# Optimization experiments

Hardware: AMD Instinct MI355X
Metric: run time of the kernel (lower is better)

The kernel has to match this reference:

```python
import jax, jax.numpy as jnp
import numpy as np

N = 100000      # nodes
E = 1600000     # edges
IN, H, OUT = 128, 128, 64
P_DROP = 0.5


def _glorot_linear(key, out_d, in_d):
    # PyG Linear default init (kaiming-uniform-ish); exact init is irrelevant for the baseline
    bound = 1.0 / np.sqrt(in_d)
    return jax.random.uniform(key, (out_d, in_d), jnp.float32, -bound, bound)


def setup_inputs() -> dict:
    key = jax.random.key(0)
    ks = jax.random.split(key, 8)
    x = jax.random.normal(ks[0], (N, IN), jnp.float32)
    edge_index = jax.random.randint(ks[1], (2, E), 0, N, dtype=jnp.int64)
    W1l = _glorot_linear(ks[2], H, IN)
    b1 = jnp.zeros((H,), jnp.float32)
    W1r = _glorot_linear(ks[3], H, IN)
    W2l = _glorot_linear(ks[4], OUT, H)
    b2 = jnp.zeros((OUT,), jnp.float32)
    W2r = _glorot_linear(ks[5], OUT, H)
    return dict(x=x, edge_index=edge_index, W1l=W1l, b1=b1, W1r=W1r,
                W2l=W2l, b2=b2, W2r=W2r)


def _sage_conv(x, src, dst, Wl, bl, Wr):
    # PyG SAGEConv (aggr='mean'): out = lin_l(mean_{j in N(i)} x_j) + lin_r(x_i)
    msg = x[src]                                             # [E, d] gather
    agg = jax.ops.segment_sum(msg, dst, num_segments=N)      # [N, d] scatter-add
    cnt = jax.ops.segment_sum(jnp.ones((src.shape[0], 1), x.dtype), dst,
                              num_segments=N)                # [N, 1] in-degree
    mean = agg / jnp.maximum(cnt, 1.0)                       # isolated nodes -> 0
    return mean @ Wl.T + bl + x @ Wr.T


def reference(x, edge_index, W1l, b1, W1r, W2l, b2, W2r):
    src, dst = edge_index[0], edge_index[1]
    h = _sage_conv(x, src, dst, W1l, b1, W1r)
    h = jax.nn.relu(h)
    # F.dropout(p=0.5) made deterministic with a fixed key
    keep = jax.random.bernoulli(jax.random.key(42), 1.0 - P_DROP, h.shape)
    h = jnp.where(keep, h / (1.0 - P_DROP), 0.0)
    return _sage_conv(h, src, dst, W2l, b2, W2r)
```

## Files before the change

kernel.cpp:

```cpp
#include <hip/hip_runtime.h>
#include <hip/hip_bf16.h>

#define N_NODES 100000
#define NE      1600000

#define BINSH 7
#define NBIN  782
#define BCAP  3072
#define SEPB  16384
#define SC_BLKS ((NE + SEPB - 1) / SEPB)
#define PRE_BLKS 512
#define NMASKW 200000

typedef __attribute__((ext_vector_type(8))) short bfrag;
typedef __attribute__((ext_vector_type(4))) float ffrag;

#define BFLO(u) __uint_as_float((u) << 16)
#define BFHI(u) __uint_as_float((u) & 0xffff0000u)

__device__ __forceinline__ unsigned tf_rotl(unsigned x, int d) {
    return (x << d) | (x >> (32 - d));
}

__device__ __forceinline__ unsigned tf_word(unsigned f) {
    const unsigned ks0 = 0u;
    const unsigned ks1 = 42u;
    const unsigned ks2 = 0x1BD11BDAu ^ 0u ^ 42u;
    unsigned x0 = 0u + ks0;
    unsigned x1 = f + ks1;
#define TF_RND(r) { x0 += x1; x1 = tf_rotl(x1, r); x1 ^= x0; }
    TF_RND(13) TF_RND(15) TF_RND(26) TF_RND(6)
    x0 += ks1; x1 += ks2 + 1u;
    TF_RND(17) TF_RND(29) TF_RND(16) TF_RND(24)
    x0 += ks2; x1 += ks0 + 2u;
    TF_RND(13) TF_RND(15) TF_RND(26) TF_RND(6)
    x0 += ks0; x1 += ks1 + 3u;
    TF_RND(17) TF_RND(29) TF_RND(16) TF_RND(24)
    x0 += ks1; x1 += ks2 + 4u;
    TF_RND(13) TF_RND(15) TF_RND(26) TF_RND(6)
    x0 += ks2; x1 += ks0 + 5u;
#undef TF_RND
    return x0 ^ x1;
}

__device__ __forceinline__ unsigned short bf_bits(float v) {
    __hip_bfloat16 b = __float2bfloat16(v);
    return *(unsigned short*)&b;
}

__global__ __launch_bounds__(1024) void k_prescatter(
    const int* __restrict__ ei, int* __restrict__ bincur, int* __restrict__ pairs,
    const float4* __restrict__ x4, ushort4* __restrict__ xb4,
    const float* __restrict__ W1l, const float* __restrict__ W1r,
    const float* __restrict__ W2l, const float* __restrict__ W2r,
    __hip_bfloat16* __restrict__ wb, unsigned long long* __restrict__ km) {
    const int t = threadIdx.x;

    if (blockIdx.x < SC_BLKS) {
        __shared__ int nz;
        __shared__ int h[NBIN];
        __shared__ int lbase[NBIN];
        if (t == 0) nz = 0;
        for (int i = t; i < NBIN; i += 1024) h[i] = 0;
        __syncthreads();
        if (t < 1024 && ei[2 * t + 1] != 0) atomicAdd(&nz, 1);
        __syncthreads();
        const int is64 = (nz == 0) ? 1 : 0;

        const int e0 = blockIdx.x * SEPB + t;
        int d[16], s[16];
#pragma unroll
        for (int k = 0; k < 16; ++k) {
            int e = e0 + k * 1024;
            if (e < NE) {
                d[k] = is64 ? ei[2 * (NE + e)] : ei[NE + e];
                s[k] = is64 ? ei[2 * e]        : ei[e];
                atomicAdd(&h[d[k] >> BINSH], 1);
            } else {
                d[k] = -1; s[k] = 0;
            }
        }
        __syncthreads();
        for (int i = t; i < NBIN; i += 1024) {
            int c = h[i];
            lbase[i] = c ? atomicAdd(&bincur[i], c) : 0;
            h[i] = 0;
        }
        __syncthreads();
#pragma unroll
        for (int k = 0; k < 16; ++k) {
            if (d[k] >= 0) {
                int b = d[k] >> BINSH;
                int r = atomicAdd(&h[b], 1);
                pairs[(size_t)b * BCAP + lbase[b] + r] =
                    ((d[k] & 127) << 17) | s[k];
            }
        }
    } else {
        const int tid0 = (blockIdx.x - SC_BLKS) * 1024 + t;
        const int stride = (PRE_BLKS - SC_BLKS) * 1024;
        for (int i = tid0; i < N_NODES * 128 / 4; i += stride) {
            float4 v = x4[i];
            ushort4 o;
            o.x = bf_bits(v.x); o.y = bf_bits(v.y);
            o.z = bf_bits(v.z); o.w = bf_bits(v.w);
            xb4[i] = o;
        }
        for (int i = tid0; i < 49152; i += stride) {
            float v;
            if (i < 16384)      v = W1l[i];
            else if (i < 32768) v = W1r[i - 16384];
            else if (i < 40960) v = W2l[i - 32768];
            else                v = W2r[i - 40960];
            wb[i] = __float2bfloat16(v);
        }
        const int lane = t & 63;
        const int gw = tid0 >> 6;
        const int nw = stride >> 6;
        for (int widx = gw; widx < NMASKW; widx += nw) {
            unsigned wv = tf_word((unsigned)widx * 64u + (unsigned)lane);
            unsigned long long keep = __ballot(!(wv & 0x80000000u));
            if (lane == 0) km[widx] = keep;
        }
    }
}

__global__ __launch_bounds__(1024) void k_aggcsr(
        const __hip_bfloat16* __restrict__ feat,
        const int* __restrict__ pairs, const int* __restrict__ bincnt,
        int* __restrict__ ptr, int* __restrict__ adj,
        __hip_bfloat16* __restrict__ mean) {
    __shared__ int ladj[BCAP];
    __shared__ int cnt[128];
    __shared__ int sc[128];
    __shared__ int woff[128];
    __shared__ int red[16];
    __shared__ int base_s;
    const int b = blockIdx.x >> 1;
    const int hb = blockIdx.x & 1;
    const int t = threadIdx.x;

    int s = 0;
    for (int i = t; i < b; i += 1024) s += bincnt[i];
#pragma unroll
    for (int off = 32; off > 0; off >>= 1) s += __shfl_down(s, off);
    if ((t & 63) == 0) red[t >> 6] = s;
    if (t < 128) cnt[t] = 0;
    __syncthreads();
    if (t == 0) {
        int tot = 0;
#pragma unroll
        for (int i = 0; i < 16; ++i) tot += red[i];
        base_s = tot;
    }
    __syncthreads();
    const int base = base_s;
    const int nb = bincnt[b];
    const int* pb = pairs + (size_t)b * BCAP;

    for (int i = t; i < nb; i += 1024)
        atomicAdd(&cnt[(pb[i] >> 17) & 127], 1);
    __syncthreads();
    if (t < 128) sc[t] = cnt[t];
    __syncthreads();
    for (int o = 1; o < 128; o <<= 1) {
        int u = 0;
        if (t < 128 && t >= o) u = sc[t - o];
        __syncthreads();
        if (t < 128) sc[t] += u;
        __syncthreads();
    }
    if (t < 128) {
        int ex = sc[t] - cnt[t];
        int node = b * 128 + t;
        if (hb == ((t >> 6) & 1) && node <= N_NODES) ptr[node] = base + ex;
        woff[t] = ex;
    }
    __syncthreads();
    for (int i = t; i < nb; i += 1024) {
        int pk = pb[i];
        int dl = (pk >> 17) & 127;
        if ((dl >> 6) == hb) {
            int r = atomicAdd(&woff[dl], 1);
            int src = pk & 0x1FFFF;
            ladj[r] = src;
            adj[base + r] = src;
        }
    }
    __syncthreads();

    const int w = t >> 6;
    const int l = t & 63;
    const int half = l >> 5;
    const size_t coff = (size_t)(l & 31) * 4;
    for (int i = 0; i < 4; ++i) {
        const int local = hb * 64 + w * 4 + i;
        const int node = b * 128 + local;
        if (node >= N_NODES) continue;
        const int p1 = sc[local];
        const int p0 = p1 - cnt[local];
        float c0 = 0.f, c1 = 0.f, c2 = 0.f, c3 = 0.f;
        float d0 = 0.f, d1 = 0.f, d2 = 0.f, d3 = 0.f;
        int p = p0;
        for (; p + 15 < p1; p += 16) {
            int sx[8];
#pragma unroll
            for (int k = 0; k < 8; ++k) sx[k] = ladj[p + 2 * k + half];
#pragma unroll
            for (int k = 0; k < 8; ++k) {
                uint2 u = *(const uint2*)(feat + (size_t)sx[k] * 128 + coff);
                if (k & 1) { d0 += BFLO(u.x); d1 += BFHI(u.x); d2 += BFLO(u.y); d3 += BFHI(u.y); }
                else       { c0 += BFLO(u.x); c1 += BFHI(u.x); c2 += BFLO(u.y); c3 += BFHI(u.y); }
            }
        }
        for (; p + 7 < p1; p += 8) {
            int sx[4];
#pragma unroll
            for (int k = 0; k < 4; ++k) sx[k] = ladj[p + 2 * k + half];
#pragma unroll
            for (int k = 0; k < 4; ++k) {
                uint2 u = *(const uint2*)(feat + (size_t)sx[k] * 128 + coff);
                if (k & 1) { d0 += BFLO(u.x); d1 += BFHI(u.x); d2 += BFLO(u.y); d3 += BFHI(u.y); }
                else       { c0 += BFLO(u.x); c1 += BFHI(u.x); c2 += BFLO(u.y); c3 += BFHI(u.y); }
            }
        }
        for (; p + 1 < p1; p += 2) {
            int sx = ladj[p + half];
            uint2 u = *(const uint2*)(feat + (size_t)sx * 128 + coff);
            c0 += BFLO(u.x); c1 += BFHI(u.x); c2 += BFLO(u.y); c3 += BFHI(u.y);
        }
        if (p < p1 && half == 0) {
            int sx = ladj[p];
            uint2 u = *(const uint2*)(feat + (size_t)sx * 128 + coff);
            c0 += BFLO(u.x); c1 += BFHI(u.x); c2 += BFLO(u.y); c3 += BFHI(u.y);
        }
        c0 += d0; c1 += d1; c2 += d2; c3 += d3;
        c0 += __shfl_xor(c0, 32);
        c1 += __shfl_xor(c1, 32);
        c2 += __shfl_xor(c2, 32);
        c3 += __shfl_xor(c3, 32);
        if (half == 0) {
            const float inv = 1.0f / (float)max(p1 - p0, 1);
            uint2 o;
            o.x = ((unsigned)bf_bits(c1 * inv) << 16) | (unsigned)bf_bits(c0 * inv);
            o.y = ((unsigned)bf_bits(c3 * inv) << 16) | (unsigned)bf_bits(c2 * inv);
            *(uint2*)(mean + (size_t)node * 128 + coff) = o;
        }
    }
}

__global__ __launch_bounds__(256) void k_lin1f(
    const __hip_bfloat16* __restrict__ Am, const __hip_bfloat16* __restrict__ Ax,
    const __hip_bfloat16* __restrict__ W1l, const __hip_bfloat16* __restrict__ W1r,
    const float* __restrict__ b1,
    const __hip_bfloat16* __restrict__ W2l, const __hip_bfloat16* __restrict__ W2r,
    const float* __restrict__ b2,
    const unsigned long long* __restrict__ kmask,
    __hip_bfloat16* __restrict__ y2, __hip_bfloat16* __restrict__ zb) {
    __shared__ __align__(16) __hip_bfloat16 hs[64][136];
    const int tid = threadIdx.x;
    const int w  = tid >> 6;
    const int l  = tid & 63;
    const int lr = l & 15;
    const int lk = l >> 4;
    const int j0 = w * 32;
    const int j2 = w * 16 + lr;
    const int n0 = blockIdx.x * 64;

    bfrag B1[2][2][4];
#pragma unroll
    for (int jt = 0; jt < 2; ++jt) {
        const int jrow = j0 + jt * 16 + lr;
#pragma unroll
        for (int ks = 0; ks < 4; ++ks) {
            B1[jt][0][ks] = *(const bfrag*)(W1l + jrow * 128 + ks * 32 + lk * 8);
            B1[jt][1][ks] = *(const bfrag*)(W1r + jrow * 128 + ks * 32 + lk * 8);
        }
    }
    bfrag Bl2[4], Br2[4];
#pragma unroll
    for (int ks = 0; ks < 4; ++ks) {
        Bl2[ks] = *(const bfrag*)(W2l + j2 * 128 + ks * 32 + lk * 8);
        Br2[ks] = *(const bfrag*)(W2r + j2 * 128 + ks * 32 + lk * 8);
    }
    const float bj0 = b1[j0 + lr];
    const float bj1 = b1[j0 + 16 + lr];
    const float bj2 = b2[j2];

    for (int t = 0; t < 4; ++t) {
        const int rbase = n0 + t * 16;
        int arow = rbase + lr;
        if (arow > N_NODES - 1) arow = N_NODES - 1;
        ffrag acc0 = {0.f, 0.f, 0.f, 0.f};
        ffrag acc1 = {0.f, 0.f, 0.f, 0.f};
#pragma unroll
        for (int ks = 0; ks < 4; ++ks) {
            bfrag am = *(const bfrag*)(Am + (size_t)arow * 128 + ks * 32 + lk * 8);
            bfrag ax = *(const bfrag*)(Ax + (size_t)arow * 128 + ks * 32 + lk * 8);
            acc0 = __builtin_amdgcn_mfma_f32_16x16x32_bf16(am, B1[0][0][ks], acc0, 0, 0, 0);
            acc1 = __builtin_amdgcn_mfma_f32_16x16x32_bf16(am, B1[1][0][ks], acc1, 0, 0, 0);
            acc0 = __builtin_amdgcn_mfma_f32_16x16x32_bf16(ax, B1[0][1][ks], acc0, 0, 0, 0);
            acc1 = __builtin_amdgcn_mfma_f32_16x16x32_bf16(ax, B1[1][1][ks], acc1, 0, 0, 0);
        }
#pragma unroll
        for (int r = 0; r < 4; ++r) {
            const int n = rbase + lk * 4 + r;
            const int lrow = t * 16 + lk * 4 + r;
            const int nm = (n < N_NODES) ? n : (N_NODES - 1);
            const unsigned long long km = kmask[nm * 2 + (j0 >> 6)];
            float v0 = fmaxf(acc0[r] + bj0, 0.f);
            v0 = ((km >> ((j0 + lr) & 63)) & 1ull) ? (v0 + v0) : 0.f;
            hs[lrow][j0 + lr] = __float2bfloat16(v0);
            float v1 = fmaxf(acc1[r] + bj1, 0.f);
            v1 = ((km >> ((j0 + 16 + lr) & 63)) & 1ull) ? (v1 + v1) : 0.f;
            hs[lrow][j0 + 16 + lr] = __float2bfloat16(v1);
        }
    }
    __syncthreads();

    for (int t = 0; t < 4; ++t) {
        ffrag accY = {0.f, 0.f, 0.f, 0.f};
        ffrag accZ = {0.f, 0.f, 0.f, 0.f};
#pragma unroll
        for (int ks = 0; ks < 4; ++ks) {
            bfrag ah = *(const bfrag*)&hs[t * 16 + lr][ks * 32 + lk * 8];
            accY = __builtin_amdgcn_mfma_f32_16x16x32_bf16(ah, Bl2[ks], accY, 0, 0, 0);
            accZ = __builtin_amdgcn_mfma_f32_16x16x32_bf16(ah, Br2[ks], accZ, 0, 0, 0);
        }
#pragma unroll
        for (int r = 0; r < 4; ++r) {
            const int n = n0 + t * 16 + lk * 4 + r;
            if (n < N_NODES) {
                y2[(size_t)n * 64 + j2] = __float2bfloat16(accY[r]);
                zb[(size_t)n * 64 + j2] = __float2bfloat16(accZ[r] + bj2);
            }
        }
    }
}

__global__ void k_agg2f(const __hip_bfloat16* __restrict__ feat,
                        const int* __restrict__ ptr, const int* __restrict__ adj,
                        const __hip_bfloat16* __restrict__ zb,
                        float* __restrict__ out) {
    const int node = (blockIdx.x * blockDim.x + threadIdx.x) >> 5;
    const int sl = threadIdx.x & 31;
    if (node >= N_NODES) return;
    const int p0 = ptr[node], p1 = ptr[node + 1];
    const int sub = sl >> 4;
    const size_t coff = (size_t)(sl & 15) * 4;
    float c0 = 0.f, c1 = 0.f, c2 = 0.f, c3 = 0.f;
    float d0 = 0.f, d1 = 0.f, d2 = 0.f, d3 = 0.f;
    int p = p0;
    for (; p + 15 < p1; p += 16) {
        int s[8];
#pragma unroll
        for (int k = 0; k < 8; ++k) s[k] = adj[p + 2 * k + sub];
#pragma unroll
        for (int k = 0; k < 8; ++k) {
            uint2 u = *(const uint2*)(feat + (size_t)s[k] * 64 + coff);
            if (k & 1) { d0 += BFLO(u.x); d1 += BFHI(u.x); d2 += BFLO(u.y); d3 += BFHI(u.y); }
            else       { c0 += BFLO(u.x); c1 += BFHI(u.x); c2 += BFLO(u.y); c3 += BFHI(u.y); }
        }
    }
    for (; p + 7 < p1; p += 8) {
        int s[4];
#pragma unroll
        for (int k = 0; k < 4; ++k) s[k] = adj[p + 2 * k + sub];
#pragma unroll
        for (int k = 0; k < 4; ++k) {
            uint2 u = *(const uint2*)(feat + (size_t)s[k] * 64 + coff);
            if (k & 1) { d0 += BFLO(u.x); d1 += BFHI(u.x); d2 += BFLO(u.y); d3 += BFHI(u.y); }
            else       { c0 += BFLO(u.x); c1 += BFHI(u.x); c2 += BFLO(u.y); c3 += BFHI(u.y); }
        }
    }
    for (; p + 1 < p1; p += 2) {
        int s = adj[p + sub];
        uint2 u = *(const uint2*)(feat + (size_t)s * 64 + coff);
        c0 += BFLO(u.x); c1 += BFHI(u.x); c2 += BFLO(u.y); c3 += BFHI(u.y);
    }
    if (p < p1 && sub == 0) {
        int s = adj[p];
        uint2 u = *(const uint2*)(feat + (size_t)s * 64 + coff);
        c0 += BFLO(u.x); c1 += BFHI(u.x); c2 += BFLO(u.y); c3 += BFHI(u.y);
    }
    c0 += d0; c1 += d1; c2 += d2; c3 += d3;
    c0 += __shfl_xor(c0, 16);
    c1 += __shfl_xor(c1, 16);
    c2 += __shfl_xor(c2, 16);
    c3 += __shfl_xor(c3, 16);
    if (sub == 0) {
        const float inv = 1.0f / (float)max(p1 - p0, 1);
        uint2 zu = *(const uint2*)(zb + (size_t)node * 64 + coff);
        float4 o;
        o.x = BFLO(zu.x) + c0 * inv;
        o.y = BFHI(zu.x) + c1 * inv;
        o.z = BFLO(zu.y) + c2 * inv;
        o.w = BFHI(zu.y) + c3 * inv;
        *(float4*)(out + (size_t)node * 64 + coff) = o;
    }
}

extern "C" void kernel_launch(void* const* d_in, const int* in_sizes, int n_in,
                              void* d_out, int out_size, void* d_ws, size_t ws_size,
                              hipStream_t stream) {
    const float* x   = (const float*)d_in[0];
    const int*   ei  = (const int*)d_in[1];
    const float* W1l = (const float*)d_in[2];
    const float* b1  = (const float*)d_in[3];
    const float* W1r = (const float*)d_in[4];
    const float* W2l = (const float*)d_in[5];
    const float* b2  = (const float*)d_in[6];
    const float* W2r = (const float*)d_in[7];
    float* out = (float*)d_out;

    char* w = (char*)d_ws;
    int* bincur = (int*)w + 64;
    int* ptr    = bincur + 1024;
    int* adj    = ptr + (N_NODES + 1);
    size_t koff = (((size_t)(64 + 1024 + N_NODES + 1 + NE)) * 4 + 255)
                  & ~(size_t)255;
    unsigned long long* kmask = (unsigned long long*)(w + koff);
    size_t foff = (koff + (size_t)NMASKW * 8 + 255) & ~(size_t)255;
    __hip_bfloat16* wb    = (__hip_bfloat16*)(w + foff);
    __hip_bfloat16* w1lb  = wb;
    __hip_bfloat16* w1rb  = wb + 16384;
    __hip_bfloat16* w2lb  = wb + 32768;
    __hip_bfloat16* w2rb  = wb + 40960;
    __hip_bfloat16* xb    = wb + 49152;
    __hip_bfloat16* meanb = xb + (size_t)N_NODES * 128;
    char* pregion = (char*)(meanb + (size_t)N_NODES * 128);
    int* pairs = (int*)pregion;
    __hip_bfloat16* y2b = (__hip_bfloat16*)pregion;
    __hip_bfloat16* zbb = y2b + (size_t)N_NODES * 64;

    hipMemsetAsync(bincur, 0, 1024 * sizeof(int), stream);

    k_prescatter<<<PRE_BLKS, 1024, 0, stream>>>(ei, bincur, pairs,
                                                (const float4*)x, (ushort4*)xb,
                                                W1l, W1r, W2l, W2r, wb, kmask);

    k_aggcsr<<<NBIN * 2, 1024, 0, stream>>>(xb, pairs, bincur, ptr, adj, meanb);

    const int nb  = (N_NODES + 63) / 64;
    const int ab2 = (N_NODES + 7) / 8;

    k_lin1f<<<nb, 256, 0, stream>>>(meanb, xb, w1lb, w1rb, b1,
                                    w2lb, w2rb, b2, kmask, y2b, zbb);
    k_agg2f<<<ab2, 256, 0, stream>>>(y2b, ptr, adj, zbb, out);
}
```

Measured before the change: 223.3 us.

## Move weight conversion and dropout mask into aggregation kernel; stage lin1f stores

Moves the bf16 weight conversion and the threefry dropout-mask generation out of the prescatter kernel into extra blocks appended to the aggregation kernel. This shortens the prescatter critical path and overlaps the mask work with the CSR aggregation. It also stages the lin1f outputs through shared memory so y2 and zb are written as coalesced 8-byte row chunks instead of scattered 2-byte stores. That costs two extra block barriers per tile and a little more shared memory.

```diff
diff --git a/kernel.cpp b/kernel.cpp
--- a/kernel.cpp
+++ b/kernel.cpp
@@ -10,6 +10,7 @@
 #define SEPB  16384
 #define SC_BLKS ((NE + SEPB - 1) / SEPB)
 #define PRE_BLKS 512
+#define AGG_EXTRA 208
 #define NMASKW 200000
 
 typedef __attribute__((ext_vector_type(8))) short bfrag;
@@ -50,10 +51,7 @@
 
 __global__ __launch_bounds__(1024) void k_prescatter(
     const int* __restrict__ ei, int* __restrict__ bincur, int* __restrict__ pairs,
-    const float4* __restrict__ x4, ushort4* __restrict__ xb4,
-    const float* __restrict__ W1l, const float* __restrict__ W1r,
-    const float* __restrict__ W2l, const float* __restrict__ W2r,
-    __hip_bfloat16* __restrict__ wb, unsigned long long* __restrict__ km) {
+    const float4* __restrict__ x4, ushort4* __restrict__ xb4) {
     const int t = threadIdx.x;
 
     if (blockIdx.x < SC_BLKS) {
@@ -106,6 +104,20 @@
             o.z = bf_bits(v.z); o.w = bf_bits(v.w);
             xb4[i] = o;
         }
+    }
+}
+
+__global__ __launch_bounds__(1024) void k_aggcsr(
+        const __hip_bfloat16* __restrict__ feat,
+        const int* __restrict__ pairs, const int* __restrict__ bincnt,
+        int* __restrict__ ptr, int* __restrict__ adj,
+        __hip_bfloat16* __restrict__ mean,
+        const float* __restrict__ W1l, const float* __restrict__ W1r,
+        const float* __restrict__ W2l, const float* __restrict__ W2r,
+        __hip_bfloat16* __restrict__ wb, unsigned long long* __restrict__ km) {
+    if (blockIdx.x >= NBIN * 2) {
+        const int tid0 = (blockIdx.x - NBIN * 2) * 1024 + threadIdx.x;
+        const int stride = AGG_EXTRA * 1024;
         for (int i = tid0; i < 49152; i += stride) {
             float v;
             if (i < 16384)      v = W1l[i];
@@ -114,7 +126,7 @@
             else                v = W2r[i - 40960];
             wb[i] = __float2bfloat16(v);
         }
-        const int lane = t & 63;
+        const int lane = threadIdx.x & 63;
         const int gw = tid0 >> 6;
         const int nw = stride >> 6;
         for (int widx = gw; widx < NMASKW; widx += nw) {
@@ -122,14 +134,9 @@
             unsigned long long keep = __ballot(!(wv & 0x80000000u));
             if (lane == 0) km[widx] = keep;
         }
-    }
-}
-
-__global__ __launch_bounds__(1024) void k_aggcsr(
-        const __hip_bfloat16* __restrict__ feat,
-        const int* __restrict__ pairs, const int* __restrict__ bincnt,
-        int* __restrict__ ptr, int* __restrict__ adj,
-        __hip_bfloat16* __restrict__ mean) {
+        return;
+    }
+
     __shared__ int ladj[BCAP];
     __shared__ int cnt[128];
     __shared__ int sc[128];
@@ -258,6 +265,8 @@
     const unsigned long long* __restrict__ kmask,
     __hip_bfloat16* __restrict__ y2, __hip_bfloat16* __restrict__ zb) {
     __shared__ __align__(16) __hip_bfloat16 hs[64][136];
+    __shared__ __align__(16) unsigned short sy[16][68];
+    __shared__ __align__(16) unsigned short sz[16][68];
     const int tid = threadIdx.x;
     const int w  = tid >> 6;
     const int l  = tid & 63;
@@ -329,12 +338,22 @@
         }
 #pragma unroll
         for (int r = 0; r < 4; ++r) {
-            const int n = n0 + t * 16 + lk * 4 + r;
+            sy[lk * 4 + r][j2] = bf_bits(accY[r]);
+            sz[lk * 4 + r][j2] = bf_bits(accZ[r] + bj2);
+        }
+        __syncthreads();
+        {
+            const int row = tid >> 4;
+            const int c4 = (tid & 15) * 4;
+            const int n = n0 + t * 16 + row;
             if (n < N_NODES) {
-                y2[(size_t)n * 64 + j2] = __float2bfloat16(accY[r]);
-                zb[(size_t)n * 64 + j2] = __float2bfloat16(accZ[r] + bj2);
+                ushort4 vy = *(const ushort4*)&sy[row][c4];
+                ushort4 vz = *(const ushort4*)&sz[row][c4];
+                *(ushort4*)((unsigned short*)y2 + (size_t)n * 64 + c4) = vy;
+                *(ushort4*)((unsigned short*)zb + (size_t)n * 64 + c4) = vz;
             }
         }
+        __syncthreads();
     }
 }
 
@@ -436,10 +455,11 @@
     hipMemsetAsync(bincur, 0, 1024 * sizeof(int), stream);
 
     k_prescatter<<<PRE_BLKS, 1024, 0, stream>>>(ei, bincur, pairs,
-                                                (const float4*)x, (ushort4*)xb,
-                                                W1l, W1r, W2l, W2r, wb, kmask);
-
-    k_aggcsr<<<NBIN * 2, 1024, 0, stream>>>(xb, pairs, bincur, ptr, adj, meanb);
+                                                (const float4*)x, (ushort4*)xb);
+
+    k_aggcsr<<<NBIN * 2 + AGG_EXTRA, 1024, 0, stream>>>(
+        xb, pairs, bincur, ptr, adj, meanb,
+        W1l, W1r, W2l, W2r, wb, kmask);
 
     const int nb  = (N_NODES + 63) / 64;
     const int ab2 = (N_NODES + 7) / 8;
```

After: 257.8 us. 1.15x slower.
